# Optimization experiments

Hardware: AMD Instinct MI355X
Metric: run time of the kernel (lower is better)

Reference implementation:

```python
import jax, jax.numpy as jnp
import numpy as np

B, S, D = 2, 2048, 4096
NH, NKV, HD = 32, 8, 128
MAX_SEQ = 2048
ROPE_THETA = 500000.0


def setup_inputs() -> dict:
    key = jax.random.key(0)
    ks = jax.random.split(key, 5)
    hidden_states = jax.random.normal(ks[0], (B, S, D), dtype=jnp.float32)
    attention_mask = jnp.ones((B, S), dtype=jnp.float32)
    position_ids = jnp.broadcast_to(jnp.arange(S, dtype=jnp.int32)[None, :], (B, S))
    wq = jax.random.normal(ks[1], (D, NH * HD), dtype=jnp.float32) * (1.0 / np.sqrt(D))
    wk = jax.random.normal(ks[2], (D, NKV * HD), dtype=jnp.float32) * (1.0 / np.sqrt(D))
    wv = jax.random.normal(ks[3], (D, NKV * HD), dtype=jnp.float32) * (1.0 / np.sqrt(D))
    wo = jax.random.normal(ks[4], (D, D), dtype=jnp.float32) * (1.0 / np.sqrt(D))
    return {"hidden_states": hidden_states, "attention_mask": attention_mask,
            "position_ids": position_ids, "wq": wq, "wk": wk, "wv": wv, "wo": wo}


def _rope_cos_sin(position_ids):
    # freqs_cis = exp(i * outer(t, inv_freq)); gathered at position_ids
    inv_freq = 1.0 / (ROPE_THETA ** (jnp.arange(0, HD, 2, dtype=jnp.float32) / HD))  # [HD/2]
    t = jnp.arange(2 * MAX_SEQ, dtype=jnp.float32)
    freqs = jnp.outer(t, inv_freq)                       # [2*MAX_SEQ, HD/2]
    cos = jnp.take(jnp.cos(freqs), position_ids, axis=0)  # [B,S,HD/2]
    sin = jnp.take(jnp.sin(freqs), position_ids, axis=0)
    return cos, sin


def _apply_rope(x, cos, sin):
    # x: [B,S,H,HD] viewed as HD/2 complex pairs; (a+bi)*(c+si)
    xr = x.astype(jnp.float32).reshape(*x.shape[:-1], -1, 2)
    a, b = xr[..., 0], xr[..., 1]
    c, s = cos[:, :, None, :], sin[:, :, None, :]
    out = jnp.stack((a * c - b * s, a * s + b * c), axis=-1)
    return out.reshape(x.shape)


def reference(hidden_states, attention_mask, position_ids, wq, wk, wv, wo):
    n_rep = NH // NKV
    xq = jnp.einsum('bsd,df->bsf', hidden_states, wq).reshape(B, S, NH, HD)
    xk = jnp.einsum('bsd,df->bsf', hidden_states, wk).reshape(B, S, NKV, HD)
    xv = jnp.einsum('bsd,df->bsf', hidden_states, wv).reshape(B, S, NKV, HD)

    cos, sin = _rope_cos_sin(position_ids)
    xq = _apply_rope(xq, cos, sin)
    xk = _apply_rope(xk, cos, sin)

    # combined causal + padding mask -> additive bias
    causal = jnp.tril(jnp.ones((S, S), dtype=bool))[None, None]          # [1,1,S,S]
    pad = (attention_mask > 0)[:, None, None, :]                          # [B,1,1,S]
    mask = jnp.logical_and(causal, pad)                                   # [B,1,S,S]
    neg = jnp.finfo(jnp.float32).min
    bias = jnp.where(mask, 0.0, neg).astype(jnp.float32)

    # GQA: repeat kv heads
    xk = jnp.repeat(xk[:, :, :, None, :], n_rep, axis=3).reshape(B, S, NH, HD)
    xv = jnp.repeat(xv[:, :, :, None, :], n_rep, axis=3).reshape(B, S, NH, HD)

    scale = 1.0 / np.sqrt(HD).astype(np.float32)
    scores = jnp.einsum('bqhd,bkhd->bhqk', xq * scale, xk) + bias         # [B,NH,S,S]
    weights = jax.nn.softmax(scores, axis=-1)
    attn = jnp.einsum('bhqk,bkhd->bqhd', weights, xv).reshape(B, S, D)
    return jnp.einsum('bsd,df->bsf', attn, wo)
```

## Files before the change

kernel.cpp:

```cpp
#include <hip/hip_runtime.h>
#include <hip/hip_bf16.h>

#define DEV __device__ __forceinline__

typedef unsigned short u16;
typedef unsigned int u32;
typedef __attribute__((ext_vector_type(8))) short s16x8;
typedef __attribute__((ext_vector_type(4))) float f32x4;

constexpr int B_  = 2, S_ = 2048, D_ = 4096, NH = 32, NKV = 8, HD = 128;
constexpr int M_  = B_ * S_;
constexpr int FQ  = 6144;
constexpr float SCALE = 0.08838834764831845f;
constexpr float LOG2E = 1.4426950408889634f;
constexpr float LOG2_THETA = 18.931568569324174f;

DEV u16 f2bf(float f) {
  u32 u = __builtin_bit_cast(u32, f);
  u32 r = u + 0x7fffu + ((u >> 16) & 1u);
  return (u16)(r >> 16);
}
DEV float bf2f(u16 h) { u32 u = ((u32)h) << 16; return __builtin_bit_cast(float, u); }

DEV void gload_lds16(const void* g, void* l) {
  __builtin_amdgcn_global_load_lds((const __attribute__((address_space(1))) u32*)g,
                                   (__attribute__((address_space(3))) u32*)l, 16, 0, 0);
}

struct alignas(8) U16x4 { u16 x, y, z, w; };

__global__ __launch_bounds__(256) void cast_f32_bf16(const float* __restrict__ src,
                                                     u16* __restrict__ dst, int n4) {
  int i = blockIdx.x * 256 + threadIdx.x;
  if (i < n4) {
    float4 v = ((const float4*)src)[i];
    U16x4 o; o.x = f2bf(v.x); o.y = f2bf(v.y); o.z = f2bf(v.z); o.w = f2bf(v.w);
    ((U16x4*)dst)[i] = o;
  }
}

__global__ __launch_bounds__(256) void transpose_cast_w(const float* __restrict__ src,
                                                        u16* __restrict__ dst, int R, int C) {
  __shared__ float tile[32][33];
  const int tx = threadIdx.x & 31, ty = threadIdx.x >> 5;
  const int c0 = blockIdx.x * 32, r0 = blockIdx.y * 32;
#pragma unroll
  for (int i = 0; i < 4; ++i)
    tile[ty + i * 8][tx] = src[(size_t)(r0 + ty + i * 8) * C + c0 + tx];
  __syncthreads();
#pragma unroll
  for (int i = 0; i < 4; ++i)
    dst[(size_t)(c0 + ty + i * 8) * R + r0 + tx] = f2bf(tile[tx][ty + i * 8]);
}

__global__ __launch_bounds__(256) void transpose_v16(const u16* __restrict__ Vb,
                                                     u16* __restrict__ Vt) {
  __shared__ u16 tile[32][33];
  const int tx = threadIdx.x & 31, ty = threadIdx.x >> 5;
  const int d0 = blockIdx.x * 32, s0 = blockIdx.y * 32;
  const size_t head = blockIdx.z;
  const u16* sp = Vb + head * (size_t)S_ * HD;
  u16* dp = Vt + head * (size_t)HD * S_;
#pragma unroll
  for (int i = 0; i < 4; ++i)
    tile[ty + i * 8][tx] = sp[(size_t)(s0 + ty + i * 8) * HD + d0 + tx];
  __syncthreads();
#pragma unroll
  for (int i = 0; i < 4; ++i)
    dp[(size_t)(d0 + ty + i * 8) * S_ + s0 + tx] = tile[tx][ty + i * 8];
}

DEV void stage_tile(const u16* __restrict__ gtile, int ldg, u16* lds, int wid, int lane) {
#pragma unroll
  for (int i = 0; i < 2; ++i) {
    int c = (i * 4 + wid) * 64 + lane;
    int row = c >> 2, slot = c & 3;
    int ss = slot ^ ((row >> 1) & 3);
    gload_lds16(gtile + (size_t)row * ldg + ss * 8, lds + (size_t)(i * 4 + wid) * 512);
  }
}

DEV s16x8 frag64(const u16* lds, int row, int hi) {
  int ss = hi ^ ((row >> 1) & 3);
  return *(const s16x8*)(lds + row * 32 + ss * 8);
}

template <bool OUT_BF16>
__global__ __launch_bounds__(256) void gemm_bt(const u16* __restrict__ A,
                                               const u16* __restrict__ Bt,
                                               void* __restrict__ Cv,
                                               int Mm, int Nn, int Kk) {
  __shared__ u16 As[2][128 * 32];
  __shared__ u16 Bs[2][128 * 32];
  const int lane = threadIdx.x & 63, wid = threadIdx.x >> 6;
  const int lo = lane & 15, hi = lane >> 4;
  const int m0 = blockIdx.y * 128, n0 = blockIdx.x * 128;
  const u16* Ag = A + (size_t)m0 * Kk;
  const u16* Bg = Bt + (size_t)n0 * Kk;
  f32x4 acc[4][4] = {};
  const int nK = Kk >> 5;
  stage_tile(Ag, Kk, As[0], wid, lane);
  stage_tile(Bg, Kk, Bs[0], wid, lane);
  __syncthreads();
  const int wm = (wid >> 1) * 64, wn = (wid & 1) * 64;
  for (int kt = 0; kt < nK; ++kt) {
    const int cur = kt & 1;
    if (kt + 1 < nK) {
      stage_tile(Ag + (kt + 1) * 32, Kk, As[cur ^ 1], wid, lane);
      stage_tile(Bg + (kt + 1) * 32, Kk, Bs[cur ^ 1], wid, lane);
    }
    s16x8 af[4], bf[4];
#pragma unroll
    for (int t = 0; t < 4; ++t) af[t] = frag64(As[cur], wm + t * 16 + lo, hi);
#pragma unroll
    for (int t = 0; t < 4; ++t) bf[t] = frag64(Bs[cur], wn + t * 16 + lo, hi);
#pragma unroll
    for (int i = 0; i < 4; ++i)
#pragma unroll
      for (int j = 0; j < 4; ++j)
        acc[i][j] = __builtin_amdgcn_mfma_f32_16x16x32_bf16(af[i], bf[j], acc[i][j], 0, 0, 0);
    __syncthreads();
  }
#pragma unroll
  for (int i = 0; i < 4; ++i)
#pragma unroll
    for (int j = 0; j < 4; ++j)
#pragma unroll
      for (int r = 0; r < 4; ++r) {
        int row = m0 + wm + i * 16 + hi * 4 + r;
        int col = n0 + wn + j * 16 + lo;
        float v = acc[i][j][r];
        if (OUT_BF16) ((u16*)Cv)[(size_t)row * Nn + col] = f2bf(v);
        else          ((float*)Cv)[(size_t)row * Nn + col] = v;
      }
}

__global__ __launch_bounds__(256) void rope_split(const u16* __restrict__ QKV,
                                                  const int* __restrict__ pos,
                                                  u16* __restrict__ Qb, u16* __restrict__ Kb,
                                                  u16* __restrict__ Vb) {
  const int row = blockIdx.x;
  const int b = row >> 11, s = row & 2047;
  const float t = (float)pos[row];
  const u16* src = QKV + (size_t)row * FQ;
  for (int idx = threadIdx.x; idx < 2560; idx += 256) {
    int j; const u16* sp; u16* dp;
    if (idx < 2048) {
      int hh = idx >> 6; j = idx & 63;
      sp = src + hh * 128 + 2 * j;
      dp = Qb + ((size_t)(b * NH + hh) * S_ + s) * HD + 2 * j;
    } else {
      int p2 = idx - 2048; int kvh = p2 >> 6; j = p2 & 63;
      sp = src + 4096 + kvh * 128 + 2 * j;
      dp = Kb + ((size_t)(b * NKV + kvh) * S_ + s) * HD + 2 * j;
    }
    float a = bf2f(sp[0]), bb = bf2f(sp[1]);
    float ang = t * exp2f(-(float)j * (LOG2_THETA / 64.0f));
    float sn, cs; sincosf(ang, &sn, &cs);
    dp[0] = f2bf(a * cs - bb * sn);
    dp[1] = f2bf(a * sn + bb * cs);
  }
  for (int idx = threadIdx.x; idx < 1024; idx += 256) {
    int kvh = idx >> 7, hd = idx & 127;
    Vb[((size_t)(b * NKV + kvh) * S_ + s) * HD + hd] = src[5120 + idx];
  }
}

__global__ __launch_bounds__(256) void attn_fwd(const u16* __restrict__ Qb,
                                                const u16* __restrict__ Kb,
                                                const u16* __restrict__ Vt,
                                                const float* __restrict__ mask,
                                                u16* __restrict__ Ob) {
  __shared__ u16 Ks[32 * 128];
  __shared__ u16 Vs[128 * 32];
  __shared__ u16 Ps[4][16 * 32];
  const int lane = threadIdx.x & 63, wid = threadIdx.x >> 6;
  const int lo = lane & 15, hi = lane >> 4;
  const int qt = blockIdx.x, bkv = blockIdx.y;
  const int b = bkv >> 3, kv = bkv & 7;
  const int h = kv * 4 + wid;
  const int q0 = qt * 16;
  const u16* Qg = Qb + ((size_t)(b * NH + h) * S_ + q0) * HD;
  const u16* Kg = Kb + (size_t)(b * NKV + kv) * S_ * HD;
  const u16* Vg = Vt + (size_t)(b * NKV + kv) * HD * S_;
  s16x8 qf[4];
#pragma unroll
  for (int c = 0; c < 4; ++c)
    qf[c] = *(const s16x8*)(Qg + (size_t)lo * HD + c * 32 + hi * 8);
  float mreg[4], lreg[4];
  f32x4 acc[8] = {};
#pragma unroll
  for (int r = 0; r < 4; ++r) { mreg[r] = -1e30f; lreg[r] = 0.f; }
  const int nt = (q0 + 47) >> 5;
  for (int t = 0; t < nt; ++t) {
    const int k0 = t * 32;
#pragma unroll
    for (int i = 0; i < 2; ++i) {
      int c = (i * 4 + wid) * 64 + lane;
      int row = c >> 4, sl = c & 15, ss = sl ^ (row & 7);
      gload_lds16(Kg + (size_t)(k0 + row) * HD + ss * 8, Ks + (size_t)(i * 4 + wid) * 512);
    }
#pragma unroll
    for (int i = 0; i < 2; ++i) {
      int c = (i * 4 + wid) * 64 + lane;
      int row = c >> 2, sl = c & 3, ss = sl ^ ((row >> 1) & 3);
      gload_lds16(Vg + (size_t)row * S_ + k0 + ss * 8, Vs + (size_t)(i * 4 + wid) * 512);
    }
    __syncthreads();
    f32x4 s0 = {}, s1 = {};
#pragma unroll
    for (int c = 0; c < 4; ++c) {
      int r0 = lo, r1 = 16 + lo;
      int sl0 = (c * 4 + hi) ^ (r0 & 7);
      int sl1 = (c * 4 + hi) ^ (r1 & 7);
      s16x8 kf0 = *(const s16x8*)(Ks + r0 * 128 + sl0 * 8);
      s16x8 kf1 = *(const s16x8*)(Ks + r1 * 128 + sl1 * 8);
      s0 = __builtin_amdgcn_mfma_f32_16x16x32_bf16(qf[c], kf0, s0, 0, 0, 0);
      s1 = __builtin_amdgcn_mfma_f32_16x16x32_bf16(qf[c], kf1, s1, 0, 0, 0);
    }
    const float mv0 = mask[b * S_ + k0 + lo];
    const float mv1 = mask[b * S_ + k0 + 16 + lo];
    u16* Pw = Ps[wid];
#pragma unroll
    for (int r = 0; r < 4; ++r) {
      const int qg = q0 + hi * 4 + r;
      float v0 = s0[r] * SCALE; if ((k0 + lo) > qg || mv0 <= 0.f) v0 = -1e30f;
      float v1 = s1[r] * SCALE; if ((k0 + 16 + lo) > qg || mv1 <= 0.f) v1 = -1e30f;
      float tm = fmaxf(v0, v1);
      tm = fmaxf(tm, __shfl_xor(tm, 1));
      tm = fmaxf(tm, __shfl_xor(tm, 2));
      tm = fmaxf(tm, __shfl_xor(tm, 4));
      tm = fmaxf(tm, __shfl_xor(tm, 8));
      float mnew = fmaxf(mreg[r], tm);
      float corr = exp2f((mreg[r] - mnew) * LOG2E);
      float p0 = exp2f((v0 - mnew) * LOG2E);
      float p1 = exp2f((v1 - mnew) * LOG2E);
      float rs = p0 + p1;
      rs += __shfl_xor(rs, 1); rs += __shfl_xor(rs, 2);
      rs += __shfl_xor(rs, 4); rs += __shfl_xor(rs, 8);
      lreg[r] = lreg[r] * corr + rs;
      mreg[r] = mnew;
#pragma unroll
      for (int n = 0; n < 8; ++n) acc[n][r] *= corr;
      const int prow = hi * 4 + r;
      const int swz = (prow >> 1) & 3;
      const int c0 = lo, c1 = 16 + lo;
      Pw[prow * 32 + ((c0 >> 3) ^ swz) * 8 + (c0 & 7)] = f2bf(p0);
      Pw[prow * 32 + ((c1 >> 3) ^ swz) * 8 + (c1 & 7)] = f2bf(p1);
    }
    {
      const int prow = lo;
      const int ss = hi ^ ((prow >> 1) & 3);
      s16x8 pa = *(const s16x8*)(Pw + prow * 32 + ss * 8);
#pragma unroll
      for (int n = 0; n < 8; ++n) {
        int vrow = n * 16 + lo;
        int vs = hi ^ ((vrow >> 1) & 3);
        s16x8 vf = *(const s16x8*)(Vs + vrow * 32 + vs * 8);
        acc[n] = __builtin_amdgcn_mfma_f32_16x16x32_bf16(pa, vf, acc[n], 0, 0, 0);
      }
    }
    __syncthreads();
  }
  float inv[4];
#pragma unroll
  for (int r = 0; r < 4; ++r) inv[r] = 1.0f / lreg[r];
#pragma unroll
  for (int n = 0; n < 8; ++n)
#pragma unroll
    for (int r = 0; r < 4; ++r) {
      int row = b * S_ + q0 + hi * 4 + r;
      int col = h * HD + n * 16 + lo;
      Ob[(size_t)row * D_ + col] = f2bf(acc[n][r] * inv[r]);
    }
}

extern "C" void kernel_launch(void* const* d_in, const int* in_sizes, int n_in,
                              void* d_out, int out_size, void* d_ws, size_t ws_size,
                              hipStream_t stream) {
  const float* X    = (const float*)d_in[0];
  const float* mask = (const float*)d_in[1];
  const int*   pos  = (const int*)d_in[2];
  const float* wq   = (const float*)d_in[3];
  const float* wk   = (const float*)d_in[4];
  const float* wv   = (const float*)d_in[5];
  const float* wo   = (const float*)d_in[6];
  float* out = (float*)d_out;
  char* ws = (char*)d_ws;

  const size_t R1 = 50331648, R2 = 50331648;
  u16* Xb  = (u16*)(ws);
  u16* Qb  = (u16*)(ws);
  u16* Kb  = (u16*)(ws + 33554432);
  u16* Vt  = (u16*)(ws + 41943040);
  u16* WT  = (u16*)(ws + R1);
  u16* WoT = (u16*)(ws + R1);
  u16* Vb  = (u16*)(ws + R1 + 33554432);
  u16* QKV = (u16*)(ws + R1 + R2);
  u16* Ab  = (u16*)(ws + R1 + R2);

  cast_f32_bf16<<<dim3(16384), dim3(256), 0, stream>>>(X, Xb, M_ * D_ / 4);
  transpose_cast_w<<<dim3(128, 128), dim3(256), 0, stream>>>(wq, WT, 4096, 4096);
  transpose_cast_w<<<dim3(32, 128),  dim3(256), 0, stream>>>(wk, WT + (size_t)4096 * 4096, 4096, 1024);
  transpose_cast_w<<<dim3(32, 128),  dim3(256), 0, stream>>>(wv, WT + (size_t)5120 * 4096, 4096, 1024);
  gemm_bt<true><<<dim3(FQ / 128, M_ / 128), dim3(256), 0, stream>>>(Xb, WT, QKV, M_, FQ, D_);
  rope_split<<<dim3(M_), dim3(256), 0, stream>>>(QKV, pos, Qb, Kb, Vb);
  transpose_v16<<<dim3(4, 64, 16), dim3(256), 0, stream>>>(Vb, Vt);
  transpose_cast_w<<<dim3(128, 128), dim3(256), 0, stream>>>(wo, WoT, 4096, 4096);
  attn_fwd<<<dim3(S_ / 16, B_ * NKV), dim3(256), 0, stream>>>(Qb, Kb, Vt, mask, Ab);
  gemm_bt<false><<<dim3(D_ / 128, M_ / 128), dim3(256), 0, stream>>>(Ab, WoT, out, M_, D_, D_);
}
```

Measured before the change: 976.1 us.

## Rewrite attention with 32x32 MFMA tiles, double-buffered KV, and lazy rescaling

Rewrites the flash-attention kernel so each block handles 32 query rows per head with 64-key tiles and 32x32x16 bf16 MFMAs, computing S^T so the probabilities stay in registers and are packed through cross-lane shuffles instead of an LDS round-trip. K/V tiles are double-buffered with async global-to-LDS loads that overlap compute. The block order is reversed so the longest causal tiles start first. Masking now runs only on the diagonal tile or when padding is present, and the running max is rescaled only when it grows by more than a threshold. This adds register pressure and relies on manual vmcnt waits and subtle lane layouts, which raises the risk of correctness mistakes.

```diff
diff --git a/kernel.cpp b/kernel.cpp
--- a/kernel.cpp
+++ b/kernel.cpp
@@ -5,14 +5,18 @@
 
 typedef unsigned short u16;
 typedef unsigned int u32;
+typedef unsigned long long u64;
 typedef __attribute__((ext_vector_type(8))) short s16x8;
 typedef __attribute__((ext_vector_type(4))) float f32x4;
+typedef __attribute__((ext_vector_type(16))) float f32x16;
+typedef __attribute__((ext_vector_type(4))) u32 u32x4;
 
 constexpr int B_  = 2, S_ = 2048, D_ = 4096, NH = 32, NKV = 8, HD = 128;
 constexpr int M_  = B_ * S_;
 constexpr int FQ  = 6144;
 constexpr float SCALE = 0.08838834764831845f;
 constexpr float LOG2E = 1.4426950408889634f;
+constexpr float C1F = SCALE * LOG2E;
 constexpr float LOG2_THETA = 18.931568569324174f;
 
 DEV u16 f2bf(float f) {
@@ -26,6 +30,14 @@
   __builtin_amdgcn_global_load_lds((const __attribute__((address_space(1))) u32*)g,
                                    (__attribute__((address_space(3))) u32*)l, 16, 0, 0);
 }
+
+DEV u32 cvtpk(float lo, float hi) {
+  u32 r;
+  asm("v_cvt_pk_bf16_f32 %0, %1, %2" : "=v"(r) : "v"(lo), "v"(hi));
+  return r;
+}
+
+DEV void cfence() { asm volatile("" ::: "memory"); }
 
 struct alignas(8) U16x4 { u16 x, y, z, w; };
 
@@ -166,113 +178,188 @@
   }
 }
 
-__global__ __launch_bounds__(256) void attn_fwd(const u16* __restrict__ Qb,
-                                                const u16* __restrict__ Kb,
-                                                const u16* __restrict__ Vt,
-                                                const float* __restrict__ mask,
-                                                u16* __restrict__ Ob) {
-  __shared__ u16 Ks[32 * 128];
-  __shared__ u16 Vs[128 * 32];
-  __shared__ u16 Ps[4][16 * 32];
+template<int KB>
+DEV void mask_tile(f32x16& st, int k0, int qg, int hs, bool padbad, float mvv) {
+#pragma unroll
+  for (int r = 0; r < 16; ++r) {
+    int kl = KB * 32 + (r & 3) + 8 * (r >> 2) + 4 * hs;
+    float s = st[r];
+    if (k0 + kl > qg) s = -1e30f;
+    if (padbad) { float mj = __shfl(mvv, kl); if (mj <= 0.f) s = -1e30f; }
+    st[r] = s;
+  }
+}
+
+DEV void stage_kv(const u16* __restrict__ Kg, const u16* __restrict__ Vg, int k0,
+                  u16* KsB, u16* VsB, int wid, int lane) {
+#pragma unroll
+  for (int i = 0; i < 4; ++i) {
+    int c = (i * 4 + wid) * 64 + lane;
+    int row = c >> 4, sl = c & 15;
+    gload_lds16(Kg + (size_t)(k0 + row) * HD + (sl ^ (row & 7)) * 8,
+                KsB + (size_t)(i * 4 + wid) * 512);
+  }
+#pragma unroll
+  for (int i = 0; i < 4; ++i) {
+    int c = (i * 4 + wid) * 64 + lane;
+    int row = c >> 3, sl = c & 7;
+    gload_lds16(Vg + (size_t)row * S_ + k0 + (sl ^ (row & 7)) * 8,
+                VsB + (size_t)(i * 4 + wid) * 512);
+  }
+}
+
+DEV s16x8 kfrag(const u16* KsB, int kb, int dblk, int lane) {
+  int row = kb * 32 + (lane & 31);
+  int sl = (2 * dblk + (lane >> 5)) ^ (row & 7);
+  return *(const s16x8*)(KsB + row * 128 + sl * 8);
+}
+DEV s16x8 vfrag(const u16* VsB, int ks, int dblk, int lane) {
+  int row = dblk * 32 + (lane & 31);
+  int sl = (2 * ks + (lane >> 5)) ^ (row & 7);
+  return *(const s16x8*)(VsB + row * 64 + sl * 8);
+}
+
+__global__ __launch_bounds__(256, 2) void attn_fwd(const u16* __restrict__ Qb,
+                                                   const u16* __restrict__ Kb,
+                                                   const u16* __restrict__ Vt,
+                                                   const float* __restrict__ mask,
+                                                   u16* __restrict__ Ob) {
+  __shared__ u16 Ks[2][64 * 128];
+  __shared__ u16 Vs[2][128 * 64];
   const int lane = threadIdx.x & 63, wid = threadIdx.x >> 6;
-  const int lo = lane & 15, hi = lane >> 4;
-  const int qt = blockIdx.x, bkv = blockIdx.y;
+  const int hs = lane >> 5;
+  const int qt = (int)gridDim.x - 1 - (int)blockIdx.x;
+  const int bkv = blockIdx.y;
   const int b = bkv >> 3, kv = bkv & 7;
   const int h = kv * 4 + wid;
-  const int q0 = qt * 16;
+  const int q0 = qt * 32;
+  const int qg = q0 + (lane & 31);
   const u16* Qg = Qb + ((size_t)(b * NH + h) * S_ + q0) * HD;
   const u16* Kg = Kb + (size_t)(b * NKV + kv) * S_ * HD;
   const u16* Vg = Vt + (size_t)(b * NKV + kv) * HD * S_;
-  s16x8 qf[4];
-#pragma unroll
-  for (int c = 0; c < 4; ++c)
-    qf[c] = *(const s16x8*)(Qg + (size_t)lo * HD + c * 32 + hi * 8);
-  float mreg[4], lreg[4];
-  f32x4 acc[8] = {};
-#pragma unroll
-  for (int r = 0; r < 4; ++r) { mreg[r] = -1e30f; lreg[r] = 0.f; }
-  const int nt = (q0 + 47) >> 5;
+
+  s16x8 qf[8];
+#pragma unroll
+  for (int dblk = 0; dblk < 8; ++dblk)
+    qf[dblk] = *(const s16x8*)(Qg + (size_t)(lane & 31) * HD + dblk * 16 + 8 * hs);
+
+  f32x16 acc[4] = {};
+  float m_run = -1e30f, mz = -1e30f, l_run = 0.f;
+  const int nt = (q0 + 95) >> 6;
+
+  stage_kv(Kg, Vg, 0, Ks[0], Vs[0], wid, lane);
+
   for (int t = 0; t < nt; ++t) {
-    const int k0 = t * 32;
-#pragma unroll
-    for (int i = 0; i < 2; ++i) {
-      int c = (i * 4 + wid) * 64 + lane;
-      int row = c >> 4, sl = c & 15, ss = sl ^ (row & 7);
-      gload_lds16(Kg + (size_t)(k0 + row) * HD + ss * 8, Ks + (size_t)(i * 4 + wid) * 512);
-    }
-#pragma unroll
-    for (int i = 0; i < 2; ++i) {
-      int c = (i * 4 + wid) * 64 + lane;
-      int row = c >> 2, sl = c & 3, ss = sl ^ ((row >> 1) & 3);
-      gload_lds16(Vg + (size_t)row * S_ + k0 + ss * 8, Vs + (size_t)(i * 4 + wid) * 512);
-    }
-    __syncthreads();
-    f32x4 s0 = {}, s1 = {};
-#pragma unroll
-    for (int c = 0; c < 4; ++c) {
-      int r0 = lo, r1 = 16 + lo;
-      int sl0 = (c * 4 + hi) ^ (r0 & 7);
-      int sl1 = (c * 4 + hi) ^ (r1 & 7);
-      s16x8 kf0 = *(const s16x8*)(Ks + r0 * 128 + sl0 * 8);
-      s16x8 kf1 = *(const s16x8*)(Ks + r1 * 128 + sl1 * 8);
-      s0 = __builtin_amdgcn_mfma_f32_16x16x32_bf16(qf[c], kf0, s0, 0, 0, 0);
-      s1 = __builtin_amdgcn_mfma_f32_16x16x32_bf16(qf[c], kf1, s1, 0, 0, 0);
-    }
-    const float mv0 = mask[b * S_ + k0 + lo];
-    const float mv1 = mask[b * S_ + k0 + 16 + lo];
-    u16* Pw = Ps[wid];
-#pragma unroll
-    for (int r = 0; r < 4; ++r) {
-      const int qg = q0 + hi * 4 + r;
-      float v0 = s0[r] * SCALE; if ((k0 + lo) > qg || mv0 <= 0.f) v0 = -1e30f;
-      float v1 = s1[r] * SCALE; if ((k0 + 16 + lo) > qg || mv1 <= 0.f) v1 = -1e30f;
-      float tm = fmaxf(v0, v1);
-      tm = fmaxf(tm, __shfl_xor(tm, 1));
-      tm = fmaxf(tm, __shfl_xor(tm, 2));
-      tm = fmaxf(tm, __shfl_xor(tm, 4));
-      tm = fmaxf(tm, __shfl_xor(tm, 8));
-      float mnew = fmaxf(mreg[r], tm);
-      float corr = exp2f((mreg[r] - mnew) * LOG2E);
-      float p0 = exp2f((v0 - mnew) * LOG2E);
-      float p1 = exp2f((v1 - mnew) * LOG2E);
-      float rs = p0 + p1;
-      rs += __shfl_xor(rs, 1); rs += __shfl_xor(rs, 2);
-      rs += __shfl_xor(rs, 4); rs += __shfl_xor(rs, 8);
-      lreg[r] = lreg[r] * corr + rs;
-      mreg[r] = mnew;
-#pragma unroll
-      for (int n = 0; n < 8; ++n) acc[n][r] *= corr;
-      const int prow = hi * 4 + r;
-      const int swz = (prow >> 1) & 3;
-      const int c0 = lo, c1 = 16 + lo;
-      Pw[prow * 32 + ((c0 >> 3) ^ swz) * 8 + (c0 & 7)] = f2bf(p0);
-      Pw[prow * 32 + ((c1 >> 3) ^ swz) * 8 + (c1 & 7)] = f2bf(p1);
-    }
-    {
-      const int prow = lo;
-      const int ss = hi ^ ((prow >> 1) & 3);
-      s16x8 pa = *(const s16x8*)(Pw + prow * 32 + ss * 8);
-#pragma unroll
-      for (int n = 0; n < 8; ++n) {
-        int vrow = n * 16 + lo;
-        int vs = hi ^ ((vrow >> 1) & 3);
-        s16x8 vf = *(const s16x8*)(Vs + vrow * 32 + vs * 8);
-        acc[n] = __builtin_amdgcn_mfma_f32_16x16x32_bf16(pa, vf, acc[n], 0, 0, 0);
+    const int k0 = t * 64;
+    const int cur = t & 1;
+    float mvv = mask[b * S_ + k0 + lane];
+    cfence();
+    __builtin_amdgcn_s_barrier();
+    if (t + 1 < nt) {
+      stage_kv(Kg, Vg, k0 + 64, Ks[cur ^ 1], Vs[cur ^ 1], wid, lane);
+      asm volatile("s_waitcnt vmcnt(8)" ::: "memory");
+    } else {
+      asm volatile("s_waitcnt vmcnt(0)" ::: "memory");
+    }
+    __builtin_amdgcn_s_barrier();
+    cfence();
+
+    const u16* KsB = Ks[cur];
+    const u16* VsB = Vs[cur];
+
+    f32x16 st0 = {}, st1 = {};
+#pragma unroll
+    for (int dblk = 0; dblk < 8; ++dblk) {
+      s16x8 kf0 = kfrag(KsB, 0, dblk, lane);
+      s16x8 kf1 = kfrag(KsB, 1, dblk, lane);
+      st0 = __builtin_amdgcn_mfma_f32_32x32x16_bf16(kf0, qf[dblk], st0, 0, 0, 0);
+      st1 = __builtin_amdgcn_mfma_f32_32x32x16_bf16(kf1, qf[dblk], st1, 0, 0, 0);
+    }
+
+    const bool padbad = (__ballot(mvv > 0.f) != ~0ull);
+    if (t == nt - 1 || padbad) {
+      mask_tile<0>(st0, k0, qg, hs, padbad, mvv);
+      mask_tile<1>(st1, k0, qg, hs, padbad, mvv);
+    }
+
+    float mx[16];
+#pragma unroll
+    for (int r = 0; r < 16; ++r) mx[r] = fmaxf(st0[r], st1[r]);
+#pragma unroll
+    for (int r = 0; r < 8; ++r) mx[r] = fmaxf(mx[r], mx[r + 8]);
+#pragma unroll
+    for (int r = 0; r < 4; ++r) mx[r] = fmaxf(mx[r], mx[r + 4]);
+    float tm = fmaxf(fmaxf(mx[0], mx[1]), fmaxf(mx[2], mx[3]));
+    float tmb = fmaxf(tm, __shfl_xor(tm, 32));
+
+    if (__any(tmb * C1F > mz + 8.f)) {
+      float mzold = mz;
+      m_run = fmaxf(m_run, tmb);
+      mz = m_run * C1F;
+      float corr = exp2f(mzold - mz);
+      l_run *= corr;
+#pragma unroll
+      for (int r = 0; r < 16; ++r) {
+        float cq = __shfl(corr, (r & 3) + 8 * (r >> 2) + 4 * hs);
+        acc[0][r] *= cq; acc[1][r] *= cq; acc[2][r] *= cq; acc[3][r] *= cq;
       }
     }
-    __syncthreads();
-  }
-  float inv[4];
-#pragma unroll
-  for (int r = 0; r < 4; ++r) inv[r] = 1.0f / lreg[r];
-#pragma unroll
-  for (int n = 0; n < 8; ++n)
-#pragma unroll
-    for (int r = 0; r < 4; ++r) {
-      int row = b * S_ + q0 + hi * 4 + r;
-      int col = h * HD + n * 16 + lo;
-      Ob[(size_t)row * D_ + col] = f2bf(acc[n][r] * inv[r]);
-    }
+
+    const float nmz = -mz;
+#pragma unroll
+    for (int r = 0; r < 16; ++r) {
+      st0[r] = exp2f(fmaf(st0[r], C1F, nmz));
+      st1[r] = exp2f(fmaf(st1[r], C1F, nmz));
+    }
+
+    float sm[8];
+#pragma unroll
+    for (int i = 0; i < 8; ++i) sm[i] = (st0[i] + st0[i + 8]) + (st1[i] + st1[i + 8]);
+#pragma unroll
+    for (int i = 0; i < 4; ++i) sm[i] += sm[i + 4];
+    float rs = (sm[0] + sm[1]) + (sm[2] + sm[3]);
+    l_run += rs + __shfl_xor(rs, 32);
+
+    s16x8 pa[4];
+#pragma unroll
+    for (int ks = 0; ks < 4; ++ks) {
+      const f32x16& src = (ks >= 2) ? st1 : st0;
+      const int o = 8 * (ks & 1);
+      u32 A0 = cvtpk(src[o + 0], src[o + 1]);
+      u32 A1 = cvtpk(src[o + 2], src[o + 3]);
+      u32 X0 = cvtpk(src[o + 4], src[o + 5]);
+      u32 X1 = cvtpk(src[o + 6], src[o + 7]);
+      u32 a0p = (u32)__shfl_xor((int)A0, 32);
+      u32 a1p = (u32)__shfl_xor((int)A1, 32);
+      u32 x0p = (u32)__shfl_xor((int)X0, 32);
+      u32 x1p = (u32)__shfl_xor((int)X1, 32);
+      u32x4 pw;
+      pw[0] = hs ? x0p : A0;
+      pw[1] = hs ? x1p : A1;
+      pw[2] = hs ? X0 : a0p;
+      pw[3] = hs ? X1 : a1p;
+      pa[ks] = __builtin_bit_cast(s16x8, pw);
+    }
+
+#pragma unroll
+    for (int dblk = 0; dblk < 4; ++dblk)
+#pragma unroll
+      for (int ks = 0; ks < 4; ++ks) {
+        s16x8 vf = vfrag(VsB, ks, dblk, lane);
+        acc[dblk] = __builtin_amdgcn_mfma_f32_32x32x16_bf16(pa[ks], vf, acc[dblk], 0, 0, 0);
+      }
+  }
+
+  const float linv = 1.0f / l_run;
+#pragma unroll
+  for (int r = 0; r < 16; ++r) {
+    const int qr = (r & 3) + 8 * (r >> 2) + 4 * hs;
+    const float lv = __shfl(linv, qr);
+    const size_t grow = (size_t)(b * S_ + q0 + qr);
+#pragma unroll
+    for (int dblk = 0; dblk < 4; ++dblk)
+      Ob[grow * D_ + h * HD + dblk * 32 + (lane & 31)] = f2bf(acc[dblk][r] * lv);
+  }
 }
 
 extern "C" void kernel_launch(void* const* d_in, const int* in_sizes, int n_in,
@@ -307,6 +394,6 @@
   rope_split<<<dim3(M_), dim3(256), 0, stream>>>(QKV, pos, Qb, Kb, Vb);
   transpose_v16<<<dim3(4, 64, 16), dim3(256), 0, stream>>>(Vb, Vt);
   transpose_cast_w<<<dim3(128, 128), dim3(256), 0, stream>>>(wo, WoT, 4096, 4096);
-  attn_fwd<<<dim3(S_ / 16, B_ * NKV), dim3(256), 0, stream>>>(Qb, Kb, Vt, mask, Ab);
+  attn_fwd<<<dim3(S_ / 32, B_ * NKV), dim3(256), 0, stream>>>(Qb, Kb, Vt, mask, Ab);
   gemm_bt<false><<<dim3(D_ / 128, M_ / 128), dim3(256), 0, stream>>>(Ab, WoT, out, M_, D_, D_);
 }
```

After: 830.6 us. -14.9%, faster.
